# Kernel optimization log

Measured on AMD Instinct MI355X. Metric: run time of the kernel, lower is better.

## Reference

```python
import jax, jax.numpy as jnp
import numpy as np

E = 1024
M = 6
GH = 256
FR = 16  # FiLM bottleneck r = max(16, E//64)


def setup_inputs() -> dict:
    key = jax.random.key(0)
    ks = jax.random.split(key, 32)
    n = lambda k, shape, std=0.02: jax.random.normal(k, shape, dtype=jnp.float32) * std
    inp = {
        "x": jax.random.normal(ks[0], (4, 2048, E), dtype=jnp.float32),
        # gate MLP E->GH->M
        "gw1": n(ks[1], (E, GH)), "gb1": jnp.zeros((GH,), jnp.float32),
        "gw2": n(ks[2], (GH, M)), "gb2": jnp.zeros((M,), jnp.float32),
        "ebias": jnp.zeros((M,), jnp.float32),
        "pm_alpha": jnp.float32(0.5),
        # expert 0: DoubleMLP E->2E->E
        "dfc_w": n(ks[3], (E, 2 * E)), "dfc_b": jnp.zeros((2 * E,), jnp.float32),
        "dproj_w": n(ks[4], (2 * E, E)), "dproj_b": jnp.zeros((E,), jnp.float32),
        # expert 1: SingleMLP E->E->E
        "sfc_w": n(ks[5], (E, E)), "sfc_b": jnp.zeros((E,), jnp.float32),
        "sproj_w": n(ks[6], (E, E)), "sproj_b": jnp.zeros((E,), jnp.float32),
        # expert 2: rank-2 perceptron
        "p2_w": n(ks[7], (2, E)), "p2_v": n(ks[8], (2, E)),
        "p2_alpha": jnp.ones((2,), jnp.float32), "p2_b": jnp.zeros((2,), jnp.float32),
        "p2_bias": jnp.zeros((E,), jnp.float32),
        # expert 3: rank-4 perceptron
        "p4_w": n(ks[9], (4, E)), "p4_v": n(ks[10], (4, E)),
        "p4_alpha": jnp.ones((4,), jnp.float32), "p4_b": jnp.zeros((4,), jnp.float32),
        "p4_bias": jnp.zeros((E,), jnp.float32),
        # expert 4: ReGLU1D
        "rg_u": n(ks[11], (E,)), "rg_a": jnp.ones((E,), jnp.float32),
        "rg_b": jnp.zeros((1,), jnp.float32), "rg_bias": jnp.zeros((E,), jnp.float32),
        # expert 5: FiLM E->FR->2E
        "fl_dw": n(ks[12], (E, FR)), "fl_db": jnp.zeros((FR,), jnp.float32),
        "fl_uw": n(ks[13], (FR, 2 * E)), "fl_ub": jnp.zeros((2 * E,), jnp.float32),
    }
    return inp


def _gelu(x):
    return jax.nn.gelu(x, approximate=False)  # torch nn.GELU default (erf)


def _rank_n(x, w, v, alpha, b, biasvec):
    # y = biasvec + sum_i alpha_i * gelu(<w_i,x> + b_i) * v_i
    s = jnp.einsum("bse,ne->bsn", x, w) + b
    g = _gelu(s)
    return jnp.einsum("bsn,ne->bse", alpha * g, v) + biasvec


def reference(x, gw1, gb1, gw2, gb2, ebias, pm_alpha,
              dfc_w, dfc_b, dproj_w, dproj_b,
              sfc_w, sfc_b, sproj_w, sproj_b,
              p2_w, p2_v, p2_alpha, p2_b, p2_bias,
              p4_w, p4_v, p4_alpha, p4_b, p4_bias,
              rg_u, rg_a, rg_b, rg_bias,
              fl_dw, fl_db, fl_uw, fl_ub):
    # gate logits [B,S,M]; tau=1.0
    gl = _gelu(x @ gw1 + gb1) @ gw2 + gb2 + ebias
    pi = jax.nn.softmax(gl, axis=-1)
    # top_k=1 sparse weights: mask to top-1 then renormalize
    _, topi = jax.lax.top_k(pi, 1)
    mask = jax.nn.one_hot(topi[..., 0], M, dtype=pi.dtype)
    w = pi * mask
    w = w / (jnp.sum(w, axis=-1, keepdims=True) + 1e-9)

    # experts (dropout = identity in eval)
    o0 = _gelu(x @ dfc_w + dfc_b) @ dproj_w + dproj_b            # DoubleMLP
    o1 = _gelu(x @ sfc_w + sfc_b) @ sproj_w + sproj_b            # SingleMLP
    o2 = _rank_n(x, p2_w, p2_v, p2_alpha, p2_b, p2_bias)          # perc2
    o3 = _rank_n(x, p4_w, p4_v, p4_alpha, p4_b, p4_bias)          # perc4
    s = x @ rg_u + rg_b[0]                                        # ReGLU1D
    o4 = jax.nn.sigmoid(s)[..., None] * (x * rg_a) + rg_bias
    t = _gelu(x @ fl_dw + fl_db)                                  # FiLM
    gb = t @ fl_uw + fl_ub
    gamma, beta = jnp.split(gb, 2, axis=-1)
    o5 = gamma * x + beta

    all_out = jnp.stack([o0, o1, o2, o3, o4, o5], axis=-1)        # [B,S,E,M]
    mixed = jnp.sum(all_out * w[..., None, :], axis=-1)
    return pm_alpha * mixed
```

## Files before the change

kernel.cpp:

```cpp
#include <hip/hip_runtime.h>
#include <math.h>


#define E 1024
#define GH 256
#define NEXP 6
#define NTOK 8192

typedef __attribute__((ext_vector_type(8))) short bf16x8;
typedef __attribute__((ext_vector_type(4))) float f32x4;

__device__ __forceinline__ float gelu_erf(float v) {
    return 0.5f * v * (1.0f + erff(v * 0.70710678118654752440f));
}

__device__ __forceinline__ unsigned short f2bf(float f) {
    union { float f; unsigned u; } c; c.f = f;
    unsigned u = c.u;
    u += 0x7fffu + ((u >> 16) & 1u);
    return (unsigned short)(u >> 16);
}

__device__ __forceinline__ float bf2f(unsigned short h) {
    union { unsigned u; float f; } c; c.u = ((unsigned)h) << 16;
    return c.f;
}

__device__ __forceinline__ float dot4(float4 a, float4 b) {
    return a.x * b.x + a.y * b.y + a.z * b.z + a.w * b.w;
}

__device__ __forceinline__ int ldso(int row, int q) {
    return row * 32 + ((q ^ ((row >> 1) & 3)) << 3);
}

__global__ __launch_bounds__(256)
void prep_kernel(const float* __restrict__ x, unsigned short* __restrict__ xh,
                 unsigned short* __restrict__ xl,
                 const float* __restrict__ gw1, unsigned short* __restrict__ w1cat,
                 const float* __restrict__ fl_dw, float* __restrict__ fl_dwT,
                 const float* __restrict__ dfc_w, unsigned short* __restrict__ dfc_wt,
                 const float* __restrict__ dproj_w, unsigned short* __restrict__ dpj_wt,
                 const float* __restrict__ sfc_w, unsigned short* __restrict__ sfc_wt,
                 const float* __restrict__ sproj_w, unsigned short* __restrict__ spj_wt) {
    __shared__ float tile[32][33];
    const int tid = threadIdx.x;
    const int tx = tid & 31, ty = tid >> 5;
    int b = blockIdx.x;
    if (b < 2048) {
        const int n4 = NTOK * E / 4;
        for (int i = b * 256 + tid; i < n4; i += 2048 * 256) {
            float4 v = reinterpret_cast<const float4*>(x)[i];
            ushort4 h, l;
            h.x = f2bf(v.x); l.x = f2bf(v.x - bf2f(h.x));
            h.y = f2bf(v.y); l.y = f2bf(v.y - bf2f(h.y));
            h.z = f2bf(v.z); l.z = f2bf(v.z - bf2f(h.z));
            h.w = f2bf(v.w); l.w = f2bf(v.w - bf2f(h.w));
            reinterpret_cast<ushort4*>(xh)[i] = h;
            reinterpret_cast<ushort4*>(xl)[i] = l;
        }
        return;
    }
    b -= 2048;
    if (b < 256) {
        const int c0 = (b & 7) * 32, r0 = (b >> 3) * 32;
#pragma unroll
        for (int i = 0; i < 4; ++i)
            tile[ty + i * 8][tx] = gw1[(size_t)(r0 + ty + i * 8) * GH + c0 + tx];
        __syncthreads();
#pragma unroll
        for (int i = 0; i < 4; ++i) {
            float v = tile[tx][ty + i * 8];
            unsigned short h = f2bf(v);
            size_t row = (size_t)(c0 + ty + i * 8) * 2048;
            w1cat[row + r0 + tx] = h;
            w1cat[row + 1024 + r0 + tx] = f2bf(v - bf2f(h));
        }
        return;
    }
    b -= 256;
    if (b < 64) {
        int idx = b * 256 + tid;
        int j = idx >> 10, k = idx & (E - 1);
        fl_dwT[idx] = fl_dw[k * 16 + j];
        return;
    }
    b -= 64;
    const float* src; unsigned short* dst; int R, C, nbx;
    if (b < 2048)      { src = dfc_w;   dst = dfc_wt; R = 1024; C = 2048; nbx = 64; }
    else if (b < 4096) { src = dproj_w; dst = dpj_wt; R = 2048; C = 1024; nbx = 32; b -= 2048; }
    else if (b < 5120) { src = sfc_w;   dst = sfc_wt; R = 1024; C = 1024; nbx = 32; b -= 4096; }
    else               { src = sproj_w; dst = spj_wt; R = 1024; C = 1024; nbx = 32; b -= 5120; }
    const int c0 = (b % nbx) * 32, r0 = (b / nbx) * 32;
#pragma unroll
    for (int i = 0; i < 4; ++i)
        tile[ty + i * 8][tx] = src[(size_t)(r0 + ty + i * 8) * C + c0 + tx];
    __syncthreads();
#pragma unroll
    for (int i = 0; i < 4; ++i)
        dst[(size_t)(c0 + ty + i * 8) * R + r0 + tx] = f2bf(tile[tx][ty + i * 8]);
}

__global__ __launch_bounds__(256)
void gate_partial_kernel(const unsigned short* __restrict__ xh,
                         const unsigned short* __restrict__ xl,
                         const unsigned short* __restrict__ w1cat,
                         float* __restrict__ hp0, float* __restrict__ hp1) {
    __shared__ __align__(16) unsigned short As[2][64 * 32];
    __shared__ __align__(16) unsigned short Bs[2][64 * 32];
    const int tid = threadIdx.x;
    const int t0 = blockIdx.y * 64, n0 = blockIdx.x * 64, z = blockIdx.z;
    const unsigned short* A = z ? xl : xh;
    float* hp = z ? hp1 : hp0;

    const int lane = tid & 63, wv = tid >> 6;
    const int wm = (wv & 1) * 32, wn = (wv >> 1) * 32;
    const int lm = lane & 15, q = lane >> 4;
    const int r0 = tid >> 2, gsl = tid & 3;
    const int g = gsl ^ ((r0 >> 1) & 3);
    const int so = r0 * 32 + gsl * 8;

    const unsigned short* pa = A + (size_t)(t0 + r0) * E + g * 8;
    const unsigned short* pb = w1cat + (size_t)(n0 + r0) * 2048 + g * 8;

    f32x4 acc[2][2];
#pragma unroll
    for (int s = 0; s < 2; ++s)
#pragma unroll
        for (int t = 0; t < 2; ++t) acc[s][t] = (f32x4){0.f, 0.f, 0.f, 0.f};

    bf16x8 ra = *(const bf16x8*)(pa);
    bf16x8 rb = *(const bf16x8*)(pb);
    *(bf16x8*)&As[0][so] = ra;
    *(bf16x8*)&Bs[0][so] = rb;

    int cur = 0, k0 = 0;
    while (true) {
        __syncthreads();
        const int kn = k0 + 32;
        if (kn < 2048) {
            ra = *(const bf16x8*)(pa + (kn & 1023));
            rb = *(const bf16x8*)(pb + kn);
        }
        bf16x8 af[2], bf[2];
#pragma unroll
        for (int s = 0; s < 2; ++s) af[s] = *(const bf16x8*)&As[cur][ldso(wm + s * 16 + lm, q)];
#pragma unroll
        for (int t = 0; t < 2; ++t) bf[t] = *(const bf16x8*)&Bs[cur][ldso(wn + t * 16 + lm, q)];
#pragma unroll
        for (int s = 0; s < 2; ++s)
#pragma unroll
            for (int t = 0; t < 2; ++t)
                acc[s][t] = __builtin_amdgcn_mfma_f32_16x16x32_bf16(af[s], bf[t], acc[s][t], 0, 0, 0);
        if (kn >= 2048) break;
        *(bf16x8*)&As[cur ^ 1][so] = ra;
        *(bf16x8*)&Bs[cur ^ 1][so] = rb;
        cur ^= 1; k0 = kn;
    }
#pragma unroll
    for (int s = 0; s < 2; ++s)
#pragma unroll
        for (int t = 0; t < 2; ++t)
#pragma unroll
            for (int rg = 0; rg < 4; ++rg) {
                int rl = wm + s * 16 + q * 4 + rg;
                int c  = wn + t * 16 + lm;
                hp[(size_t)(t0 + rl) * GH + n0 + c] = acc[s][t][rg];
            }
}

__global__ __launch_bounds__(256)
void gate_finalize_kernel(const float* __restrict__ hp0, const float* __restrict__ hp1,
                          const float* __restrict__ gb1, const float* __restrict__ gw2,
                          const float* __restrict__ gb2, const float* __restrict__ ebias,
                          const float* __restrict__ pm_alpha,
                          float* __restrict__ scale, int* __restrict__ counts,
                          int* __restrict__ tlist, int* __restrict__ eid) {
    __shared__ float hs[32][264];
    __shared__ float g2s[GH * NEXP];
    __shared__ int tokexp[32];
    const int tid = threadIdx.x;
    const int t0 = blockIdx.x * 32;
    for (int i = tid; i < GH * NEXP; i += 256) g2s[i] = gw2[i];
#pragma unroll
    for (int i = 0; i < 8; ++i) {
        int f4 = i * 256 + tid;
        int row = f4 >> 6, c4 = (f4 & 63) * 4;
        size_t base = (size_t)(t0 + row) * GH + c4;
        float4 a = *reinterpret_cast<const float4*>(&hp0[base]);
        float4 b = *reinterpret_cast<const float4*>(&hp1[base]);
        float4 o;
        o.x = gelu_erf(a.x + b.x + gb1[c4 + 0]);
        o.y = gelu_erf(a.y + b.y + gb1[c4 + 1]);
        o.z = gelu_erf(a.z + b.z + gb1[c4 + 2]);
        o.w = gelu_erf(a.w + b.w + gb1[c4 + 3]);
        *reinterpret_cast<float4*>(&hs[row][c4]) = o;
    }
    __syncthreads();
    const int t = tid >> 3, j = tid & 7;
    float p[NEXP] = {0.f, 0.f, 0.f, 0.f, 0.f, 0.f};
#pragma unroll 8
    for (int kk = 0; kk < 32; ++kk) {
        int k = j + kk * 8;
        float hv = hs[t][k];
        const float* gr = &g2s[k * NEXP];
#pragma unroll
        for (int m = 0; m < NEXP; ++m) p[m] += hv * gr[m];
    }
#pragma unroll
    for (int m = 0; m < NEXP; ++m) {
        p[m] += __shfl_xor(p[m], 4, 64);
        p[m] += __shfl_xor(p[m], 2, 64);
        p[m] += __shfl_xor(p[m], 1, 64);
    }
    if (j == 0) {
        float L[NEXP];
#pragma unroll
        for (int m = 0; m < NEXP; ++m) L[m] = p[m] + gb2[m] + ebias[m];
        float mx = L[0]; int am = 0;
#pragma unroll
        for (int m = 1; m < NEXP; ++m) { if (L[m] > mx) { mx = L[m]; am = m; } }
        float S = 0.f;
#pragma unroll
        for (int m = 0; m < NEXP; ++m) S += expf(L[m] - mx);
        float pt = 1.f / S;
        scale[t0 + t] = pm_alpha[0] * (pt / (pt + 1e-9f));
        eid[t0 + t] = am;
        tokexp[t] = am;
    }
    __syncthreads();
    if (tid < NEXP) {
        const int e = tid;
        int cnt = 0;
#pragma unroll
        for (int i = 0; i < 32; ++i) cnt += (tokexp[i] == e);
        if (cnt) {
            int base = atomicAdd(&counts[e], cnt);
            int pos = 0;
#pragma unroll
            for (int i = 0; i < 32; ++i)
                if (tokexp[i] == e) tlist[e * NTOK + base + (pos++)] = t0 + i;
        }
    }
}

__global__ __launch_bounds__(256)
void moe_gemm1_kernel(const unsigned short* __restrict__ xh,
                      const unsigned short* __restrict__ B0, const unsigned short* __restrict__ B1,
                      const float* __restrict__ bias0, const float* __restrict__ bias1,
                      const int* __restrict__ counts, const int* __restrict__ tlist,
                      unsigned short* __restrict__ H0, unsigned short* __restrict__ H1) {
    const int z = blockIdx.z;
    const int N = z ? 1024 : 2048;
    const int cnt = counts[z];
    const int i0 = blockIdx.y * 64;
    const int n0 = blockIdx.x * 64;
    if (i0 >= cnt || n0 >= N) return;
    const unsigned short* Bz = z ? B1 : B0;
    const float* bias = z ? bias1 : bias0;

    __shared__ __align__(16) unsigned short As[2][64 * 32];
    __shared__ __align__(16) unsigned short Bs[2][64 * 32];
    __shared__ int toks[64];
    const int tid = threadIdx.x;
    if (tid < 64) toks[tid] = tlist[z * NTOK + min(i0 + tid, cnt - 1)];
    __syncthreads();

    const int lane = tid & 63, wv = tid >> 6;
    const int wm = (wv & 1) * 32, wn = (wv >> 1) * 32;
    const int lm = lane & 15, q = lane >> 4;
    const int r0 = tid >> 2, gsl = tid & 3;
    const int g = gsl ^ ((r0 >> 1) & 3);
    const int so = r0 * 32 + gsl * 8;

    const unsigned short* pa = xh + (size_t)toks[r0] * E + g * 8;
    const unsigned short* pb = Bz + (size_t)(n0 + r0) * E + g * 8;

    f32x4 acc[2][2];
#pragma unroll
    for (int s = 0; s < 2; ++s)
#pragma unroll
        for (int t = 0; t < 2; ++t) acc[s][t] = (f32x4){0.f, 0.f, 0.f, 0.f};

    bf16x8 ra = *(const bf16x8*)(pa);
    bf16x8 rb = *(const bf16x8*)(pb);
    *(bf16x8*)&As[0][so] = ra;
    *(bf16x8*)&Bs[0][so] = rb;

    int cur = 0, k0 = 0;
    while (true) {
        __syncthreads();
        const int kn = k0 + 32;
        if (kn < E) {
            ra = *(const bf16x8*)(pa + kn);
            rb = *(const bf16x8*)(pb + kn);
        }
        bf16x8 af[2], bf[2];
#pragma unroll
        for (int s = 0; s < 2; ++s) af[s] = *(const bf16x8*)&As[cur][ldso(wm + s * 16 + lm, q)];
#pragma unroll
        for (int t = 0; t < 2; ++t) bf[t] = *(const bf16x8*)&Bs[cur][ldso(wn + t * 16 + lm, q)];
#pragma unroll
        for (int s = 0; s < 2; ++s)
#pragma unroll
            for (int t = 0; t < 2; ++t)
                acc[s][t] = __builtin_amdgcn_mfma_f32_16x16x32_bf16(af[s], bf[t], acc[s][t], 0, 0, 0);
        if (kn >= E) break;
        *(bf16x8*)&As[cur ^ 1][so] = ra;
        *(bf16x8*)&Bs[cur ^ 1][so] = rb;
        cur ^= 1; k0 = kn;
    }
    unsigned short* Hz = z ? H1 : H0;
#pragma unroll
    for (int s = 0; s < 2; ++s)
#pragma unroll
        for (int t = 0; t < 2; ++t)
#pragma unroll
            for (int rg = 0; rg < 4; ++rg) {
                int rl = wm + s * 16 + q * 4 + rg;
                int gc = n0 + wn + t * 16 + lm;
                float v = acc[s][t][rg] + bias[gc];
                Hz[(size_t)(i0 + rl) * N + gc] = f2bf(gelu_erf(v));
            }
}

__global__ __launch_bounds__(256)
void gemm2_cheap_kernel(const unsigned short* __restrict__ h1, const unsigned short* __restrict__ h2,
                        const unsigned short* __restrict__ dpj, const unsigned short* __restrict__ spj,
                        const float* __restrict__ dproj_b, const float* __restrict__ sproj_b,
                        const int* __restrict__ counts, const int* __restrict__ tlist,
                        const float* __restrict__ scale,
                        const float* __restrict__ x, const int* __restrict__ eid,
                        const float* __restrict__ p2_w, const float* __restrict__ p2_v,
                        const float* __restrict__ p2_alpha, const float* __restrict__ p2_b,
                        const float* __restrict__ p2_bias,
                        const float* __restrict__ p4_w, const float* __restrict__ p4_v,
                        const float* __restrict__ p4_alpha, const float* __restrict__ p4_b,
                        const float* __restrict__ p4_bias,
                        const float* __restrict__ rg_u, const float* __restrict__ rg_a,
                        const float* __restrict__ rg_b, const float* __restrict__ rg_bias,
                        const float* __restrict__ fl_dwT, const float* __restrict__ fl_db,
                        const float* __restrict__ fl_uw, const float* __restrict__ fl_ub,
                        float* __restrict__ out) {
    __shared__ __align__(16) char smem[2 * 64 * 32 * 2 * 2 + 64 * 4];
    const int tid = threadIdx.x;
    const int bb = blockIdx.x;
    const int lane = tid & 63;

    if (bb < 1024) {
        const int z = bb >> 9;
        const int r = bb & 511;
        const int n0 = (r & 15) * 64;
        const int i0 = (r >> 4) * 64;
        const int K = z ? 1024 : 2048;
        const int cnt = counts[z];
        if (i0 >= cnt) return;
        const int rows = min(64, cnt - i0);
        const unsigned short* Az = z ? h2 : h1;
        const unsigned short* Bz = z ? spj : dpj;
        const float* bias = z ? sproj_b : dproj_b;

        unsigned short (*As)[64 * 32] = (unsigned short (*)[64 * 32])smem;
        unsigned short (*Bs)[64 * 32] = (unsigned short (*)[64 * 32])(smem + 2 * 64 * 32 * 2);
        int* toks = (int*)(smem + 2 * 64 * 32 * 2 * 2);
        if (tid < 64) toks[tid] = tlist[z * NTOK + min(i0 + tid, cnt - 1)];
        __syncthreads();

        const int wv = tid >> 6;
        const int wm = (wv & 1) * 32, wn = (wv >> 1) * 32;
        const int lm = lane & 15, q = lane >> 4;
        const int r0 = tid >> 2, gsl = tid & 3;
        const int g = gsl ^ ((r0 >> 1) & 3);
        const int so = r0 * 32 + gsl * 8;

        const unsigned short* pa = Az + (size_t)(i0 + r0) * K + g * 8;
        const unsigned short* pb = Bz + (size_t)(n0 + r0) * K + g * 8;

        f32x4 acc[2][2];
#pragma unroll
        for (int s = 0; s < 2; ++s)
#pragma unroll
            for (int t = 0; t < 2; ++t) acc[s][t] = (f32x4){0.f, 0.f, 0.f, 0.f};

        bf16x8 ra = *(const bf16x8*)(pa);
        bf16x8 rb = *(const bf16x8*)(pb);
        *(bf16x8*)&As[0][so] = ra;
        *(bf16x8*)&Bs[0][so] = rb;

        int cur = 0, k0 = 0;
        while (true) {
            __syncthreads();
            const int kn = k0 + 32;
            if (kn < K) {
                ra = *(const bf16x8*)(pa + kn);
                rb = *(const bf16x8*)(pb + kn);
            }
            bf16x8 af[2], bf[2];
#pragma unroll
            for (int s = 0; s < 2; ++s) af[s] = *(const bf16x8*)&As[cur][ldso(wm + s * 16 + lm, q)];
#pragma unroll
            for (int t = 0; t < 2; ++t) bf[t] = *(const bf16x8*)&Bs[cur][ldso(wn + t * 16 + lm, q)];
#pragma unroll
            for (int s = 0; s < 2; ++s)
#pragma unroll
                for (int t = 0; t < 2; ++t)
                    acc[s][t] = __builtin_amdgcn_mfma_f32_16x16x32_bf16(af[s], bf[t], acc[s][t], 0, 0, 0);
            if (kn >= K) break;
            *(bf16x8*)&As[cur ^ 1][so] = ra;
            *(bf16x8*)&Bs[cur ^ 1][so] = rb;
            cur ^= 1; k0 = kn;
        }
#pragma unroll
        for (int s = 0; s < 2; ++s)
#pragma unroll
            for (int t = 0; t < 2; ++t)
#pragma unroll
                for (int rg = 0; rg < 4; ++rg) {
                    int rl = wm + s * 16 + q * 4 + rg;
                    if (rl < rows) {
                        int gc = n0 + wn + t * 16 + lm;
                        int tok = toks[rl];
                        out[(size_t)tok * E + gc] = scale[tok] * (acc[s][t][rg] + bias[gc]);
                    }
                }
        return;
    }

    const int tok = bb - 1024;
    const int e = eid[tok];
    if (e < 2) return;
    float* red = (float*)smem;
    float* gs  = red + 64;
    const int k4 = tid * 4;
    const float4 xv = *reinterpret_cast<const float4*>(&x[(size_t)tok * E + k4]);
    const float sc = scale[tok];
    const int wid = tid >> 6;
    float4 o;

    if (e == 2 || e == 3) {
        const int n = (e == 2) ? 2 : 4;
        const float* w    = (e == 2) ? p2_w : p4_w;
        const float* v    = (e == 2) ? p2_v : p4_v;
        const float* al   = (e == 2) ? p2_alpha : p4_alpha;
        const float* b    = (e == 2) ? p2_b : p4_b;
        const float* bias = (e == 2) ? p2_bias : p4_bias;
        for (int j = 0; j < n; ++j) {
            float val = dot4(xv, *reinterpret_cast<const float4*>(&w[j * E + k4]));
            for (int off = 32; off > 0; off >>= 1) val += __shfl_down(val, off, 64);
            if (lane == 0) red[j * 4 + wid] = val;
        }
        __syncthreads();
        if (tid < n) {
            float s = red[tid * 4] + red[tid * 4 + 1] + red[tid * 4 + 2] + red[tid * 4 + 3] + b[tid];
            gs[tid] = al[tid] * gelu_erf(s);
        }
        __syncthreads();
        o = *reinterpret_cast<const float4*>(&bias[k4]);
        for (int j = 0; j < n; ++j) {
            float4 vv = *reinterpret_cast<const float4*>(&v[j * E + k4]);
            float gj = gs[j];
            o.x += gj * vv.x; o.y += gj * vv.y; o.z += gj * vv.z; o.w += gj * vv.w;
        }
    } else if (e == 4) {
        float val = dot4(xv, *reinterpret_cast<const float4*>(&rg_u[k4]));
        for (int off = 32; off > 0; off >>= 1) val += __shfl_down(val, off, 64);
        if (lane == 0) red[wid] = val;
        __syncthreads();
        float s = red[0] + red[1] + red[2] + red[3] + rg_b[0];
        float sg = 1.f / (1.f + expf(-s));
        float4 av = *reinterpret_cast<const float4*>(&rg_a[k4]);
        float4 bv = *reinterpret_cast<const float4*>(&rg_bias[k4]);
        o.x = sg * xv.x * av.x + bv.x;
        o.y = sg * xv.y * av.y + bv.y;
        o.z = sg * xv.z * av.z + bv.z;
        o.w = sg * xv.w * av.w + bv.w;
    } else {
#pragma unroll
        for (int j = 0; j < 16; ++j) {
            float val = dot4(xv, *reinterpret_cast<const float4*>(&fl_dwT[j * E + k4]));
            for (int off = 32; off > 0; off >>= 1) val += __shfl_down(val, off, 64);
            if (lane == 0) red[j * 4 + wid] = val;
        }
        __syncthreads();
        if (tid < 16)
            gs[tid] = gelu_erf(red[tid * 4] + red[tid * 4 + 1] + red[tid * 4 + 2] + red[tid * 4 + 3] + fl_db[tid]);
        __syncthreads();
        float4 ga = *reinterpret_cast<const float4*>(&fl_ub[k4]);
        float4 be = *reinterpret_cast<const float4*>(&fl_ub[E + k4]);
#pragma unroll
        for (int j = 0; j < 16; ++j) {
            float tj = gs[j];
            float4 ug = *reinterpret_cast<const float4*>(&fl_uw[(size_t)j * 2 * E + k4]);
            float4 ub = *reinterpret_cast<const float4*>(&fl_uw[(size_t)j * 2 * E + E + k4]);
            ga.x += tj * ug.x; ga.y += tj * ug.y; ga.z += tj * ug.z; ga.w += tj * ug.w;
            be.x += tj * ub.x; be.y += tj * ub.y; be.z += tj * ub.z; be.w += tj * ub.w;
        }
        o.x = ga.x * xv.x + be.x;
        o.y = ga.y * xv.y + be.y;
        o.z = ga.z * xv.z + be.z;
        o.w = ga.w * xv.w + be.w;
    }
    o.x *= sc; o.y *= sc; o.z *= sc; o.w *= sc;
    *reinterpret_cast<float4*>(&out[(size_t)tok * E + k4]) = o;
}

extern "C" void kernel_launch(void* const* d_in, const int* in_sizes, int n_in,
                              void* d_out, int out_size, void* d_ws, size_t ws_size,
                              hipStream_t stream) {
    const float* x        = (const float*)d_in[0];
    const float* gw1      = (const float*)d_in[1];
    const float* gb1      = (const float*)d_in[2];
    const float* gw2      = (const float*)d_in[3];
    const float* gb2      = (const float*)d_in[4];
    const float* ebias    = (const float*)d_in[5];
    const float* pm_alpha = (const float*)d_in[6];
    const float* dfc_w    = (const float*)d_in[7];
    const float* dfc_b    = (const float*)d_in[8];
    const float* dproj_w  = (const float*)d_in[9];
    const float* dproj_b  = (const float*)d_in[10];
    const float* sfc_w    = (const float*)d_in[11];
    const float* sfc_b    = (const float*)d_in[12];
    const float* sproj_w  = (const float*)d_in[13];
    const float* sproj_b  = (const float*)d_in[14];
    const float* p2_w     = (const float*)d_in[15];
    const float* p2_v     = (const float*)d_in[16];
    const float* p2_alpha = (const float*)d_in[17];
    const float* p2_b     = (const float*)d_in[18];
    const float* p2_bias  = (const float*)d_in[19];
    const float* p4_w     = (const float*)d_in[20];
    const float* p4_v     = (const float*)d_in[21];
    const float* p4_alpha = (const float*)d_in[22];
    const float* p4_b     = (const float*)d_in[23];
    const float* p4_bias  = (const float*)d_in[24];
    const float* rg_u     = (const float*)d_in[25];
    const float* rg_a     = (const float*)d_in[26];
    const float* rg_b     = (const float*)d_in[27];
    const float* rg_bias  = (const float*)d_in[28];
    const float* fl_dw    = (const float*)d_in[29];
    const float* fl_db    = (const float*)d_in[30];
    const float* fl_uw    = (const float*)d_in[31];
    const float* fl_ub    = (const float*)d_in[32];
    float* out = (float*)d_out;

    char* ws = (char*)d_ws;
    size_t off = 0;
    int*            counts = (int*)(ws + off);            off += 256;
    float*          scale  = (float*)(ws + off);          off += (size_t)NTOK * 4;
    int*            tlist  = (int*)(ws + off);            off += (size_t)NEXP * NTOK * 4;
    int*            eid    = (int*)(ws + off);            off += (size_t)NTOK * 4;
    float*          fl_dwT = (float*)(ws + off);          off += (size_t)16 * E * 4;
    unsigned short* w1cat  = (unsigned short*)(ws + off); off += (size_t)GH * 2048 * 2;
    unsigned short* dfc_wt = (unsigned short*)(ws + off); off += (size_t)2048 * 1024 * 2;
    unsigned short* dpj_wt = (unsigned short*)(ws + off); off += (size_t)1024 * 2048 * 2;
    unsigned short* sfc_wt = (unsigned short*)(ws + off); off += (size_t)1024 * 1024 * 2;
    unsigned short* spj_wt = (unsigned short*)(ws + off); off += (size_t)1024 * 1024 * 2;
    unsigned short* x_hi   = (unsigned short*)(ws + off); off += (size_t)NTOK * E * 2;
    char* U = ws + off;
    unsigned short* x_lo = (unsigned short*)U;
    float*          hp0  = (float*)(U + (size_t)16 * 1024 * 1024);
    float*          hp1  = (float*)(U + (size_t)24 * 1024 * 1024);
    unsigned short* h1   = (unsigned short*)U;
    unsigned short* h2   = (unsigned short*)(U + (size_t)16 * 1024 * 1024);

    hipMemsetAsync(counts, 0, 256, stream);
    prep_kernel<<<8512, 256, 0, stream>>>(x, x_hi, x_lo, gw1, w1cat, fl_dw, fl_dwT,
                                          dfc_w, dfc_wt, dproj_w, dpj_wt,
                                          sfc_w, sfc_wt, sproj_w, spj_wt);
    gate_partial_kernel<<<dim3(GH / 64, NTOK / 64, 2), 256, 0, stream>>>(x_hi, x_lo, w1cat, hp0, hp1);
    gate_finalize_kernel<<<NTOK / 32, 256, 0, stream>>>(hp0, hp1, gb1, gw2, gb2, ebias,
                                                        pm_alpha, scale, counts, tlist, eid);
    moe_gemm1_kernel<<<dim3(32, 32, 2), 256, 0, stream>>>(
        x_hi, dfc_wt, sfc_wt, dfc_b, sfc_b, counts, tlist, h1, h2);
    gemm2_cheap_kernel<<<1024 + NTOK, 256, 0, stream>>>(
        h1, h2, dpj_wt, spj_wt, dproj_b, sproj_b, counts, tlist, scale,
        x, eid,
        p2_w, p2_v, p2_alpha, p2_b, p2_bias,
        p4_w, p4_v, p4_alpha, p4_b, p4_bias,
        rg_u, rg_a, rg_b, rg_bias,
        fl_dwT, fl_db, fl_uw, fl_ub, out);
    (void)in_sizes; (void)n_in; (void)out_size; (void)ws_size;
}
```

Baseline: 299.4 us.

## Fuse cheap-expert projections into gate GEMM via extra MFMA columns

```diff
diff --git a/kernel.cpp b/kernel.cpp
--- a/kernel.cpp
+++ b/kernel.cpp
@@ -6,6 +6,7 @@
 #define GH 256
 #define NEXP 6
 #define NTOK 8192
+#define NCH 24
 
 typedef __attribute__((ext_vector_type(8))) short bf16x8;
 typedef __attribute__((ext_vector_type(4))) float f32x4;
@@ -26,10 +27,6 @@
     return c.f;
 }
 
-__device__ __forceinline__ float dot4(float4 a, float4 b) {
-    return a.x * b.x + a.y * b.y + a.z * b.z + a.w * b.w;
-}
-
 __device__ __forceinline__ int ldso(int row, int q) {
     return row * 32 + ((q ^ ((row >> 1) & 3)) << 3);
 }
@@ -38,7 +35,9 @@
 void prep_kernel(const float* __restrict__ x, unsigned short* __restrict__ xh,
                  unsigned short* __restrict__ xl,
                  const float* __restrict__ gw1, unsigned short* __restrict__ w1cat,
-                 const float* __restrict__ fl_dw, float* __restrict__ fl_dwT,
+                 const float* __restrict__ p2_w, const float* __restrict__ p4_w,
+                 const float* __restrict__ rg_u, const float* __restrict__ fl_dw,
+                 unsigned short* __restrict__ w1cheap,
                  const float* __restrict__ dfc_w, unsigned short* __restrict__ dfc_wt,
                  const float* __restrict__ dproj_w, unsigned short* __restrict__ dpj_wt,
                  const float* __restrict__ sfc_w, unsigned short* __restrict__ sfc_wt,
@@ -80,9 +79,26 @@
     }
     b -= 256;
     if (b < 64) {
-        int idx = b * 256 + tid;
-        int j = idx >> 10, k = idx & (E - 1);
-        fl_dwT[idx] = fl_dw[k * 16 + j];
+        const int r = b;
+        const int k4 = tid * 4;
+        float4 v = {0.f, 0.f, 0.f, 0.f};
+        if (r < 2)       v = *reinterpret_cast<const float4*>(&p2_w[r * E + k4]);
+        else if (r < 6)  v = *reinterpret_cast<const float4*>(&p4_w[(r - 2) * E + k4]);
+        else if (r == 6) v = *reinterpret_cast<const float4*>(&rg_u[k4]);
+        else if (r < 23) {
+            const int j = r - 7;
+            v.x = fl_dw[(k4 + 0) * 16 + j];
+            v.y = fl_dw[(k4 + 1) * 16 + j];
+            v.z = fl_dw[(k4 + 2) * 16 + j];
+            v.w = fl_dw[(k4 + 3) * 16 + j];
+        }
+        ushort4 h, l;
+        h.x = f2bf(v.x); l.x = f2bf(v.x - bf2f(h.x));
+        h.y = f2bf(v.y); l.y = f2bf(v.y - bf2f(h.y));
+        h.z = f2bf(v.z); l.z = f2bf(v.z - bf2f(h.z));
+        h.w = f2bf(v.w); l.w = f2bf(v.w - bf2f(h.w));
+        *reinterpret_cast<ushort4*>(&w1cheap[r * 2048 + k4]) = h;
+        *reinterpret_cast<ushort4*>(&w1cheap[r * 2048 + 1024 + k4]) = l;
         return;
     }
     b -= 64;
@@ -105,13 +121,16 @@
 void gate_partial_kernel(const unsigned short* __restrict__ xh,
                          const unsigned short* __restrict__ xl,
                          const unsigned short* __restrict__ w1cat,
-                         float* __restrict__ hp0, float* __restrict__ hp1) {
+                         const unsigned short* __restrict__ w1cheap,
+                         float* __restrict__ hp0, float* __restrict__ hp1,
+                         float* __restrict__ cdot0, float* __restrict__ cdot1) {
     __shared__ __align__(16) unsigned short As[2][64 * 32];
     __shared__ __align__(16) unsigned short Bs[2][64 * 32];
     const int tid = threadIdx.x;
     const int t0 = blockIdx.y * 64, n0 = blockIdx.x * 64, z = blockIdx.z;
     const unsigned short* A = z ? xl : xh;
     float* hp = z ? hp1 : hp0;
+    float* cd = z ? cdot1 : cdot0;
 
     const int lane = tid & 63, wv = tid >> 6;
     const int wm = (wv & 1) * 32, wn = (wv >> 1) * 32;
@@ -123,14 +142,23 @@
     const unsigned short* pa = A + (size_t)(t0 + r0) * E + g * 8;
     const unsigned short* pb = w1cat + (size_t)(n0 + r0) * 2048 + g * 8;
 
+    const bool docheap = (blockIdx.x == 0);
+    const int tc = wv >> 1;
+    const unsigned short* pcw = w1cheap + (size_t)(tc * 16 + lm) * 2048 + q * 8;
+
     f32x4 acc[2][2];
 #pragma unroll
     for (int s = 0; s < 2; ++s)
 #pragma unroll
         for (int t = 0; t < 2; ++t) acc[s][t] = (f32x4){0.f, 0.f, 0.f, 0.f};
+    f32x4 accC[2];
+    accC[0] = (f32x4){0.f, 0.f, 0.f, 0.f};
+    accC[1] = (f32x4){0.f, 0.f, 0.f, 0.f};
 
     bf16x8 ra = *(const bf16x8*)(pa);
     bf16x8 rb = *(const bf16x8*)(pb);
+    bf16x8 cfv, cfn;
+    if (docheap) cfv = *(const bf16x8*)(pcw);
     *(bf16x8*)&As[0][so] = ra;
     *(bf16x8*)&Bs[0][so] = rb;
 
@@ -141,6 +169,7 @@
         if (kn < 2048) {
             ra = *(const bf16x8*)(pa + (kn & 1023));
             rb = *(const bf16x8*)(pb + kn);
+            if (docheap) cfn = *(const bf16x8*)(pcw + kn);
         }
         bf16x8 af[2], bf[2];
 #pragma unroll
@@ -152,9 +181,14 @@
 #pragma unroll
             for (int t = 0; t < 2; ++t)
                 acc[s][t] = __builtin_amdgcn_mfma_f32_16x16x32_bf16(af[s], bf[t], acc[s][t], 0, 0, 0);
+        if (docheap) {
+            accC[0] = __builtin_amdgcn_mfma_f32_16x16x32_bf16(af[0], cfv, accC[0], 0, 0, 0);
+            accC[1] = __builtin_amdgcn_mfma_f32_16x16x32_bf16(af[1], cfv, accC[1], 0, 0, 0);
+        }
         if (kn >= 2048) break;
         *(bf16x8*)&As[cur ^ 1][so] = ra;
         *(bf16x8*)&Bs[cur ^ 1][so] = rb;
+        cfv = cfn;
         cur ^= 1; k0 = kn;
     }
 #pragma unroll
@@ -167,6 +201,18 @@
                 int c  = wn + t * 16 + lm;
                 hp[(size_t)(t0 + rl) * GH + n0 + c] = acc[s][t][rg];
             }
+    if (docheap) {
+        const int c = tc * 16 + lm;
+        if (c < NCH) {
+#pragma unroll
+            for (int s = 0; s < 2; ++s)
+#pragma unroll
+                for (int rg = 0; rg < 4; ++rg) {
+                    int rl = wm + s * 16 + q * 4 + rg;
+                    cd[(size_t)(t0 + rl) * NCH + c] = accC[s][rg];
+                }
+        }
+    }
 }
 
 __global__ __launch_bounds__(256)
@@ -174,8 +220,13 @@
                           const float* __restrict__ gb1, const float* __restrict__ gw2,
                           const float* __restrict__ gb2, const float* __restrict__ ebias,
                           const float* __restrict__ pm_alpha,
+                          const float* __restrict__ cdot0, const float* __restrict__ cdot1,
+                          const float* __restrict__ p2_alpha, const float* __restrict__ p2_b,
+                          const float* __restrict__ p4_alpha, const float* __restrict__ p4_b,
+                          const float* __restrict__ rg_b, const float* __restrict__ fl_db,
                           float* __restrict__ scale, int* __restrict__ counts,
-                          int* __restrict__ tlist, int* __restrict__ eid) {
+                          int* __restrict__ tlist, int* __restrict__ eid,
+                          float* __restrict__ gvec) {
     __shared__ float hs[32][264];
     __shared__ float g2s[GH * NEXP];
     __shared__ int tokexp[32];
@@ -241,6 +292,18 @@
             for (int i = 0; i < 32; ++i)
                 if (tokexp[i] == e) tlist[e * NTOK + base + (pos++)] = t0 + i;
         }
+    }
+    for (int i = tid; i < 32 * NCH; i += 256) {
+        const int tt = i / NCH, slot = i - tt * NCH;
+        const int tok = t0 + tt;
+        float s = cdot0[(size_t)tok * NCH + slot] + cdot1[(size_t)tok * NCH + slot];
+        float val;
+        if (slot < 2)       val = p2_alpha[slot] * gelu_erf(s + p2_b[slot]);
+        else if (slot < 6)  val = p4_alpha[slot - 2] * gelu_erf(s + p4_b[slot - 2]);
+        else if (slot == 6) val = 1.f / (1.f + expf(-(s + rg_b[0])));
+        else if (slot < 23) val = gelu_erf(s + fl_db[slot - 7]);
+        else                val = 0.f;
+        gvec[(size_t)tok * NCH + slot] = val;
     }
 }
 
@@ -331,15 +394,10 @@
                         const int* __restrict__ counts, const int* __restrict__ tlist,
                         const float* __restrict__ scale,
                         const float* __restrict__ x, const int* __restrict__ eid,
-                        const float* __restrict__ p2_w, const float* __restrict__ p2_v,
-                        const float* __restrict__ p2_alpha, const float* __restrict__ p2_b,
-                        const float* __restrict__ p2_bias,
-                        const float* __restrict__ p4_w, const float* __restrict__ p4_v,
-                        const float* __restrict__ p4_alpha, const float* __restrict__ p4_b,
-                        const float* __restrict__ p4_bias,
-                        const float* __restrict__ rg_u, const float* __restrict__ rg_a,
-                        const float* __restrict__ rg_b, const float* __restrict__ rg_bias,
-                        const float* __restrict__ fl_dwT, const float* __restrict__ fl_db,
+                        const float* __restrict__ gvec,
+                        const float* __restrict__ p2_v, const float* __restrict__ p2_bias,
+                        const float* __restrict__ p4_v, const float* __restrict__ p4_bias,
+                        const float* __restrict__ rg_a, const float* __restrict__ rg_bias,
                         const float* __restrict__ fl_uw, const float* __restrict__ fl_ub,
                         float* __restrict__ out) {
     __shared__ __align__(16) char smem[2 * 64 * 32 * 2 * 2 + 64 * 4];
@@ -429,45 +487,31 @@
     const int tok = bb - 1024;
     const int e = eid[tok];
     if (e < 2) return;
-    float* red = (float*)smem;
-    float* gs  = red + 64;
+    const float sc = scale[tok];
     const int k4 = tid * 4;
-    const float4 xv = *reinterpret_cast<const float4*>(&x[(size_t)tok * E + k4]);
-    const float sc = scale[tok];
-    const int wid = tid >> 6;
+    const float* gv = &gvec[(size_t)tok * NCH];
     float4 o;
 
-    if (e == 2 || e == 3) {
-        const int n = (e == 2) ? 2 : 4;
-        const float* w    = (e == 2) ? p2_w : p4_w;
-        const float* v    = (e == 2) ? p2_v : p4_v;
-        const float* al   = (e == 2) ? p2_alpha : p4_alpha;
-        const float* b    = (e == 2) ? p2_b : p4_b;
-        const float* bias = (e == 2) ? p2_bias : p4_bias;
-        for (int j = 0; j < n; ++j) {
-            float val = dot4(xv, *reinterpret_cast<const float4*>(&w[j * E + k4]));
-            for (int off = 32; off > 0; off >>= 1) val += __shfl_down(val, off, 64);
-            if (lane == 0) red[j * 4 + wid] = val;
-        }
-        __syncthreads();
-        if (tid < n) {
-            float s = red[tid * 4] + red[tid * 4 + 1] + red[tid * 4 + 2] + red[tid * 4 + 3] + b[tid];
-            gs[tid] = al[tid] * gelu_erf(s);
-        }
-        __syncthreads();
-        o = *reinterpret_cast<const float4*>(&bias[k4]);
-        for (int j = 0; j < n; ++j) {
-            float4 vv = *reinterpret_cast<const float4*>(&v[j * E + k4]);
-            float gj = gs[j];
+    if (e == 2) {
+        const float g0 = gv[0], g1 = gv[1];
+        float4 b0 = *reinterpret_cast<const float4*>(&p2_bias[k4]);
+        float4 v0 = *reinterpret_cast<const float4*>(&p2_v[k4]);
+        float4 v1 = *reinterpret_cast<const float4*>(&p2_v[E + k4]);
+        o.x = b0.x + g0 * v0.x + g1 * v1.x;
+        o.y = b0.y + g0 * v0.y + g1 * v1.y;
+        o.z = b0.z + g0 * v0.z + g1 * v1.z;
+        o.w = b0.w + g0 * v0.w + g1 * v1.w;
+    } else if (e == 3) {
+        o = *reinterpret_cast<const float4*>(&p4_bias[k4]);
+#pragma unroll
+        for (int j = 0; j < 4; ++j) {
+            const float gj = gv[2 + j];
+            float4 vv = *reinterpret_cast<const float4*>(&p4_v[j * E + k4]);
             o.x += gj * vv.x; o.y += gj * vv.y; o.z += gj * vv.z; o.w += gj * vv.w;
         }
     } else if (e == 4) {
-        float val = dot4(xv, *reinterpret_cast<const float4*>(&rg_u[k4]));
-        for (int off = 32; off > 0; off >>= 1) val += __shfl_down(val, off, 64);
-        if (lane == 0) red[wid] = val;
-        __syncthreads();
-        float s = red[0] + red[1] + red[2] + red[3] + rg_b[0];
-        float sg = 1.f / (1.f + expf(-s));
+        const float sg = gv[6];
+        float4 xv = *reinterpret_cast<const float4*>(&x[(size_t)tok * E + k4]);
         float4 av = *reinterpret_cast<const float4*>(&rg_a[k4]);
         float4 bv = *reinterpret_cast<const float4*>(&rg_bias[k4]);
         o.x = sg * xv.x * av.x + bv.x;
@@ -475,21 +519,12 @@
         o.z = sg * xv.z * av.z + bv.z;
         o.w = sg * xv.w * av.w + bv.w;
     } else {
-#pragma unroll
-        for (int j = 0; j < 16; ++j) {
-            float val = dot4(xv, *reinterpret_cast<const float4*>(&fl_dwT[j * E + k4]));
-            for (int off = 32; off > 0; off >>= 1) val += __shfl_down(val, off, 64);
-            if (lane == 0) red[j * 4 + wid] = val;
-        }
-        __syncthreads();
-        if (tid < 16)
-            gs[tid] = gelu_erf(red[tid * 4] + red[tid * 4 + 1] + red[tid * 4 + 2] + red[tid * 4 + 3] + fl_db[tid]);
-        __syncthreads();
+        float4 xv = *reinterpret_cast<const float4*>(&x[(size_t)tok * E + k4]);
         float4 ga = *reinterpret_cast<const float4*>(&fl_ub[k4]);
         float4 be = *reinterpret_cast<const float4*>(&fl_ub[E + k4]);
 #pragma unroll
         for (int j = 0; j < 16; ++j) {
-            float tj = gs[j];
+            const float tj = gv[7 + j];
             float4 ug = *reinterpret_cast<const float4*>(&fl_uw[(size_t)j * 2 * E + k4]);
             float4 ub = *reinterpret_cast<const float4*>(&fl_uw[(size_t)j * 2 * E + E + k4]);
             ga.x += tj * ug.x; ga.y += tj * ug.y; ga.z += tj * ug.z; ga.w += tj * ug.w;
@@ -548,7 +583,8 @@
     float*          scale  = (float*)(ws + off);          off += (size_t)NTOK * 4;
     int*            tlist  = (int*)(ws + off);            off += (size_t)NEXP * NTOK * 4;
     int*            eid    = (int*)(ws + off);            off += (size_t)NTOK * 4;
-    float*          fl_dwT = (float*)(ws + off);          off += (size_t)16 * E * 4;
+    float*          gvec   = (float*)(ws + off);          off += (size_t)NTOK * NCH * 4;
+    unsigned short* w1cheap= (unsigned short*)(ws + off); off += (size_t)64 * 2048 * 2;
     unsigned short* w1cat  = (unsigned short*)(ws + off); off += (size_t)GH * 2048 * 2;
     unsigned short* dfc_wt = (unsigned short*)(ws + off); off += (size_t)2048 * 1024 * 2;
     unsigned short* dpj_wt = (unsigned short*)(ws + off); off += (size_t)1024 * 2048 * 2;
@@ -561,22 +597,26 @@
     float*          hp1  = (float*)(U + (size_t)24 * 1024 * 1024);
     unsigned short* h1   = (unsigned short*)U;
     unsigned short* h2   = (unsigned short*)(U + (size_t)16 * 1024 * 1024);
+    float* cdot0 = out;
+    float* cdot1 = out + (size_t)NTOK * NCH;
 
     hipMemsetAsync(counts, 0, 256, stream);
-    prep_kernel<<<8512, 256, 0, stream>>>(x, x_hi, x_lo, gw1, w1cat, fl_dw, fl_dwT,
+    prep_kernel<<<8512, 256, 0, stream>>>(x, x_hi, x_lo, gw1, w1cat,
+                                          p2_w, p4_w, rg_u, fl_dw, w1cheap,
                                           dfc_w, dfc_wt, dproj_w, dpj_wt,
                                           sfc_w, sfc_wt, sproj_w, spj_wt);
-    gate_partial_kernel<<<dim3(GH / 64, NTOK / 64, 2), 256, 0, stream>>>(x_hi, x_lo, w1cat, hp0, hp1);
-    gate_finalize_kernel<<<NTOK / 32, 256, 0, stream>>>(hp0, hp1, gb1, gw2, gb2, ebias,
-                                                        pm_alpha, scale, counts, tlist, eid);
+    gate_partial_kernel<<<dim3(GH / 64, NTOK / 64, 2), 256, 0, stream>>>(
+        x_hi, x_lo, w1cat, w1cheap, hp0, hp1, cdot0, cdot1);
+    gate_finalize_kernel<<<NTOK / 32, 256, 0, stream>>>(
+        hp0, hp1, gb1, gw2, gb2, ebias, pm_alpha, cdot0, cdot1,
+        p2_alpha, p2_b, p4_alpha, p4_b, rg_b, fl_db,
+        scale, counts, tlist, eid, gvec);
     moe_gemm1_kernel<<<dim3(32, 32, 2), 256, 0, stream>>>(
         x_hi, dfc_wt, sfc_wt, dfc_b, sfc_b, counts, tlist, h1, h2);
     gemm2_cheap_kernel<<<1024 + NTOK, 256, 0, stream>>>(
         h1, h2, dpj_wt, spj_wt, dproj_b, sproj_b, counts, tlist, scale,
-        x, eid,
-        p2_w, p2_v, p2_alpha, p2_b, p2_bias,
-        p4_w, p4_v, p4_alpha, p4_b, p4_bias,
-        rg_u, rg_a, rg_b, rg_bias,
-        fl_dwT, fl_db, fl_uw, fl_ub, out);
+        x, eid, gvec,
+        p2_v, p2_bias, p4_v, p4_bias,
+        rg_a, rg_bias, fl_uw, fl_ub, out);
     (void)in_sizes; (void)n_in; (void)out_size; (void)ws_size;
 }
```

After: 304.0 us. Within noise of the previous version (+1.5%).
